# Performance work log

Measured on AMD Instinct MI355X. Metric: run time of the kernel, lower is better.

The kernel has to match this reference:

```python
import jax, jax.numpy as jnp
import numpy as np

B, Q, K, D, H = 2, 2048, 2048, 1024, 16
HD = D // H  # 64
EPS = 1e-6  # flax LayerNorm default epsilon


def setup_inputs() -> dict:
    key = jax.random.key(0)
    ks = jax.random.split(key, 12)
    s = 1.0 / np.sqrt(D)  # lecun_normal-like scale
    inputs_q = jax.random.normal(ks[0], (B, Q, D), jnp.float32)
    bias = jax.random.normal(ks[1], (B, 1, Q, K), jnp.float32)
    mask = jax.random.randint(ks[2], (B, 1, Q, K), 0, 2).astype(jnp.bool_)
    wq = jax.random.normal(ks[3], (D, H, HD), jnp.float32) * s
    wk = jax.random.normal(ks[4], (D, H, HD), jnp.float32) * s
    wv = jax.random.normal(ks[5], (D, H, HD), jnp.float32) * s
    bq = jnp.zeros((H, HD), jnp.float32)
    bk = jnp.zeros((H, HD), jnp.float32)
    bv = jnp.zeros((H, HD), jnp.float32)
    q_scale = jnp.ones((HD,), jnp.float32)
    k_scale = jnp.ones((HD,), jnp.float32)
    wo = jax.random.normal(ks[6], (H, HD, D), jnp.float32) * s
    bo = jnp.zeros((D,), jnp.float32)
    return dict(inputs_q=inputs_q, bias=bias, mask=mask, wq=wq, bq=bq,
                wk=wk, bk=bk, wv=wv, bv=bv, q_scale=q_scale, k_scale=k_scale,
                wo=wo, bo=bo)


def _layernorm_nobias(x, scale):
    # normalize over last axis (head_dim), no bias, like flax LayerNorm(use_bias=False)
    mean = jnp.mean(x, axis=-1, keepdims=True)
    var = jnp.mean(jnp.square(x - mean), axis=-1, keepdims=True)
    return (x - mean) * jax.lax.rsqrt(var + EPS) * scale


def reference(inputs_q, bias, mask, wq, bq, wk, bk, wv, bv, q_scale, k_scale, wo, bo):
    # QKV projections (self-attention: k and v inputs default to inputs_q)
    q = jnp.einsum('bqd,dhe->bqhe', inputs_q, wq) + bq  # [B,Q,H,HD]
    k = jnp.einsum('bkd,dhe->bkhe', inputs_q, wk) + bk  # [B,K,H,HD]
    v = jnp.einsum('bkd,dhe->bkhe', inputs_q, wv) + bv  # [B,K,H,HD]
    # optional QK layernorm (normalize_qk=True)
    q = _layernorm_nobias(q, q_scale)
    k = _layernorm_nobias(k, k_scale)
    # attention weights
    q = q / jnp.sqrt(jnp.asarray(q.shape[-1], q.dtype))
    attn = jnp.einsum('bqhe,bkhe->bhqk', q, k)  # [B,H,Q,K]
    attn = attn + bias
    big_neg = jnp.finfo(q.dtype).min
    attn = jnp.where(mask, attn, big_neg)
    attn = jax.nn.softmax(attn.astype(jnp.float32), axis=-1).astype(q.dtype)
    # weighted values + output projection
    x = jnp.einsum('bhqk,bkhe->bqhe', attn, v)  # [B,Q,H,HD]
    out = jnp.einsum('bqhe,heo->bqo', x, wo) + bo  # [B,Q,D]
    return out
```

## Files before the change

### kernel.cpp

```cpp
#include <hip/hip_runtime.h>
#include <cstdint>
#include <cstddef>

typedef __bf16 bf16_t;
typedef __bf16 bf16x8 __attribute__((ext_vector_type(8)));
typedef __bf16 bf16x4 __attribute__((ext_vector_type(4)));
typedef _Float16 f16_t;
typedef _Float16 f16x4 __attribute__((ext_vector_type(4)));
typedef float f32x4 __attribute__((ext_vector_type(4)));

constexpr int BB = 2, SS = 2048, DD = 1024, HH = 16, HDIM = 64;
constexpr int BS = BB * SS;
constexpr float LOG2E = 1.4426950408889634f;

__device__ __forceinline__ void glds16(const void* g, void* l) {
  __builtin_amdgcn_global_load_lds((const __attribute__((address_space(1))) void*)g,
                                   (__attribute__((address_space(3))) void*)l, 16, 0, 0);
}

__global__ __launch_bounds__(256) void prep_fused(
    const float* __restrict__ x, const float* __restrict__ wq, const float* __restrict__ wk,
    const float* __restrict__ wv, const float* __restrict__ wo, const float* __restrict__ bias,
    const int* __restrict__ mask, bf16_t* __restrict__ xb, bf16_t* __restrict__ wqkv_t,
    bf16_t* __restrict__ wo_t, bf16_t* __restrict__ bmq) {
  __shared__ float tile[64][65];
  int bid = blockIdx.x;
  int t = threadIdx.x;
  if (bid < 4096) {
    int i = bid * 256 + t;
    float4 v = ((const float4*)x)[i];
    union { bf16_t h[4]; uint2 u; } o;
    o.h[0] = (bf16_t)v.x; o.h[1] = (bf16_t)v.y; o.h[2] = (bf16_t)v.z; o.h[3] = (bf16_t)v.w;
    ((uint2*)xb)[i] = o.u;
  } else if (bid < 5120) {
    int id = bid - 4096;
    int which = id >> 8, tr = (id >> 4) & 15, tc = id & 15;
    const float* src = (which == 0) ? wq : (which == 1) ? wk : (which == 2) ? wv : wo;
    bf16_t* dst = (which < 3) ? wqkv_t : wo_t;
    int noff = (which < 3) ? which * 1024 : 0;
#pragma unroll
    for (int p = 0; p < 4; ++p) {
      int e = (p * 256 + t) * 4;
      int r = e >> 6, c = e & 63;
      float4 v = *(const float4*)&src[(size_t)(tr * 64 + r) * 1024 + tc * 64 + c];
      tile[r][c] = v.x; tile[r][c + 1] = v.y; tile[r][c + 2] = v.z; tile[r][c + 3] = v.w;
    }
    __syncthreads();
#pragma unroll
    for (int p = 0; p < 4; ++p) {
      int e = (p * 256 + t) * 4;
      int r = e >> 6, c = e & 63;
      union { bf16_t h[4]; uint2 u; } o;
#pragma unroll
      for (int j = 0; j < 4; ++j) o.h[j] = (bf16_t)tile[c + j][r];
      *(uint2*)&dst[(size_t)(noff + tc * 64 + r) * 1024 + tr * 64 + c] = o.u;
    }
  } else {
    int i = (bid - 5120) * 256 + t;
    float4 b0 = ((const float4*)bias)[i * 2];
    float4 b1 = ((const float4*)bias)[i * 2 + 1];
    int4 m0 = ((const int4*)mask)[i * 2];
    int4 m1 = ((const int4*)mask)[i * 2 + 1];
    union { bf16_t h[8]; uint4 u; } o;
    o.h[0] = (bf16_t)(m0.x ? b0.x * LOG2E - 8.0f : -2.0e38f);
    o.h[1] = (bf16_t)(m0.y ? b0.y * LOG2E - 8.0f : -2.0e38f);
    o.h[2] = (bf16_t)(m0.z ? b0.z * LOG2E - 8.0f : -2.0e38f);
    o.h[3] = (bf16_t)(m0.w ? b0.w * LOG2E - 8.0f : -2.0e38f);
    o.h[4] = (bf16_t)(m1.x ? b1.x * LOG2E - 8.0f : -2.0e38f);
    o.h[5] = (bf16_t)(m1.y ? b1.y * LOG2E - 8.0f : -2.0e38f);
    o.h[6] = (bf16_t)(m1.z ? b1.z * LOG2E - 8.0f : -2.0e38f);
    o.h[7] = (bf16_t)(m1.w ? b1.w * LOG2E - 8.0f : -2.0e38f);
    ((uint4*)bmq)[i] = o.u;
  }
}

template <bool OUT_F32>
__global__ __launch_bounds__(256) void gemm_bt(const bf16_t* __restrict__ A,
                                               const bf16_t* __restrict__ Bt,
                                               bf16_t* __restrict__ Cb, float* __restrict__ Cf,
                                               const float* __restrict__ bias, int M, int N,
                                               int Kd) {
  __shared__ __align__(16) bf16_t As[128][32];
  __shared__ __align__(16) bf16_t Bs[128][32];
  int tid = threadIdx.x;
  int lane = tid & 63, w = tid >> 6;
  int lo = lane & 15, quad = lane >> 4;
  int wm = w >> 1, wn = w & 1;
  int m0 = blockIdx.y * 128, n0 = blockIdx.x * 128;
  int srow = lane >> 2;
  int scol = (lane & 3) * 8;
  f32x4 acc[4][4] = {};
  for (int kk = 0; kk < Kd; kk += 32) {
#pragma unroll
    for (int t = 0; t < 2; ++t) {
      int rb = (w * 2 + t) * 16;
      glds16(&A[(size_t)(m0 + rb + srow) * Kd + kk + scol], &As[rb][0]);
      glds16(&Bt[(size_t)(n0 + rb + srow) * Kd + kk + scol], &Bs[rb][0]);
    }
    asm volatile("s_waitcnt vmcnt(0)" ::: "memory");
    __syncthreads();
    bf16x8 am[4], bn[4];
#pragma unroll
    for (int i = 0; i < 4; ++i) am[i] = *(const bf16x8*)&As[wm * 64 + i * 16 + lo][quad * 8];
#pragma unroll
    for (int i = 0; i < 4; ++i) bn[i] = *(const bf16x8*)&Bs[wn * 64 + i * 16 + lo][quad * 8];
#pragma unroll
    for (int mi = 0; mi < 4; ++mi)
#pragma unroll
      for (int ni = 0; ni < 4; ++ni)
        acc[mi][ni] = __builtin_amdgcn_mfma_f32_16x16x32_bf16(am[mi], bn[ni], acc[mi][ni], 0, 0, 0);
    __syncthreads();
  }
#pragma unroll
  for (int mi = 0; mi < 4; ++mi) {
#pragma unroll
    for (int ni = 0; ni < 4; ++ni) {
#pragma unroll
      for (int r = 0; r < 4; ++r) {
        int row = m0 + wm * 64 + mi * 16 + quad * 4 + r;
        int col = n0 + wn * 64 + ni * 16 + lo;
        float v = acc[mi][ni][r];
        if (OUT_F32)
          Cf[(size_t)row * N + col] = v + bias[col];
        else
          Cb[(size_t)row * N + col] = (bf16_t)v;
      }
    }
  }
}

__global__ __launch_bounds__(256) void postqkv(const bf16_t* __restrict__ Cqkv,
                                               const float* __restrict__ bq,
                                               const float* __restrict__ bk,
                                               const float* __restrict__ bv,
                                               const float* __restrict__ q_scale,
                                               const float* __restrict__ k_scale,
                                               bf16_t* __restrict__ qb, bf16_t* __restrict__ kb,
                                               f16_t* __restrict__ vt) {
  __shared__ float tile[64][65];
  int bid = blockIdx.x;
  int t = threadIdx.x;
  if (bid < 32768) {
    int mode = bid >> 14;
    int vec = (bid & 16383) * 4 + (t >> 6);
    int lane = t & 63;
    int bs = vec >> 4, h = vec & 15;
    int b = bs >> 11, s = bs & 2047;
    const float* badd = (mode == 0) ? bq : bk;
    float x = (float)Cqkv[(size_t)bs * 3072 + mode * 1024 + h * 64 + lane] + badd[h * 64 + lane];
    float sum = x;
#pragma unroll
    for (int off = 32; off >= 1; off >>= 1) sum += __shfl_xor(sum, off, 64);
    float mean = sum * (1.0f / 64.0f);
    float d = x - mean;
    float vs = d * d;
#pragma unroll
    for (int off = 32; off >= 1; off >>= 1) vs += __shfl_xor(vs, off, 64);
    float var = vs * (1.0f / 64.0f);
    const float* sc = (mode == 0) ? q_scale : k_scale;
    float y = d * rsqrtf(var + 1e-6f) * sc[lane];
    if (mode == 0) y *= 0.125f * LOG2E;
    bf16_t* dst = (mode == 0) ? qb : kb;
    dst[(size_t)((b * 16 + h) * 2048 + s) * 64 + lane] = (bf16_t)y;
  } else {
    int id2 = bid - 32768;
    int st = id2 & 31, h = (id2 >> 5) & 15, b = id2 >> 9;
#pragma unroll
    for (int p = 0; p < 2; ++p) {
      int e = (p * 256 + t) * 8;
      int r = e >> 6, c = e & 63;
      bf16x8 v8 = *(const bf16x8*)&Cqkv[(size_t)(b * SS + st * 64 + r) * 3072 + 2048 + h * 64 + c];
#pragma unroll
      for (int j = 0; j < 8; ++j) tile[r][c + j] = (float)v8[j] + bv[h * 64 + c + j];
    }
    __syncthreads();
#pragma unroll
    for (int p = 0; p < 2; ++p) {
      int e = (p * 256 + t) * 8;
      int r = e >> 6, c = e & 63;
      union { f16_t h[8]; uint4 u; } o;
#pragma unroll
      for (int j = 0; j < 8; ++j) o.h[j] = (f16_t)tile[c + j][r];
      *(uint4*)&vt[(size_t)((b * HH + h) * HDIM + r) * SS + st * 64 + c] = o.u;
    }
  }
}

__global__ __launch_bounds__(256) void attn_kernel(const bf16_t* __restrict__ qb,
                                                   const bf16_t* __restrict__ kb,
                                                   const f16_t* __restrict__ vt,
                                                   const bf16_t* __restrict__ bmq,
                                                   bf16_t* __restrict__ xout) {
  __shared__ __align__(16) bf16_t Ks[64][72];
  __shared__ __align__(16) f16_t Vs[64][72];
  __shared__ __align__(16) bf16_t Bm[128][72];
  int tid = threadIdx.x;
  int lane = tid & 63, w = tid >> 6;
  int lo = lane & 15, quad = lane >> 4;
  int qt = blockIdx.x, h = blockIdx.y, b = blockIdx.z;
  size_t headoff = (size_t)(b * HH + h) * SS * HDIM;
  int q0b = qt * 128;
  int q0 = q0b + w * 32;
  const bf16_t* kbase = kb + headoff;
  const f16_t* vbase = vt + headoff;
  const bf16_t* bmbase = bmq + (size_t)b * SS * SS;

  bf16x8 bqf[2][2];
#pragma unroll
  for (int qg = 0; qg < 2; ++qg)
#pragma unroll
    for (int ec = 0; ec < 2; ++ec)
      bqf[qg][ec] =
          *(const bf16x8*)&qb[headoff + (size_t)(q0 + qg * 16 + lo) * HDIM + ec * 32 + quad * 8];

  f16x4 ones;
#pragma unroll
  for (int j = 0; j < 4; ++j) ones[j] = (f16_t)1.0f;

  f32x4 ot[2][4] = {};
  f32x4 lacc[2] = {};

  for (int kt = 0; kt < SS / 64; ++kt) {
    int k0 = kt * 64;
#pragma unroll
    for (int p = 0; p < 2; ++p) {
      int idx = (p * 256 + tid) * 8;
      int r = idx >> 6, c = idx & 63;
      *(uint4*)&Ks[r][c] = *(const uint4*)&kbase[(size_t)(k0 + r) * HDIM + c];
      *(uint4*)&Vs[r][c] = *(const uint4*)&vbase[(size_t)r * SS + k0 + c];
    }
#pragma unroll
    for (int p = 0; p < 4; ++p) {
      int idx = (p * 256 + tid) * 8;
      int r = idx >> 6, c = idx & 63;
      *(uint4*)&Bm[r][c] = *(const uint4*)&bmbase[(size_t)(q0b + r) * SS + k0 + c];
    }
    __syncthreads();

    bf16x8 ka[4][2];
#pragma unroll
    for (int mb = 0; mb < 4; ++mb)
#pragma unroll
      for (int ec = 0; ec < 2; ++ec)
        ka[mb][ec] = *(const bf16x8*)&Ks[mb * 16 + lo][ec * 32 + quad * 8];

    f16x4 pf[2][4];
#pragma unroll
    for (int qg = 0; qg < 2; ++qg) {
#pragma unroll
      for (int mb = 0; mb < 4; ++mb) {
        bf16x4 bm4 = *(const bf16x4*)&Bm[w * 32 + qg * 16 + lo][mb * 16 + quad * 4];
        f32x4 s;
#pragma unroll
        for (int r = 0; r < 4; ++r) s[r] = (float)bm4[r];
        s = __builtin_amdgcn_mfma_f32_16x16x32_bf16(ka[mb][0], bqf[qg][0], s, 0, 0, 0);
        s = __builtin_amdgcn_mfma_f32_16x16x32_bf16(ka[mb][1], bqf[qg][1], s, 0, 0, 0);
#pragma unroll
        for (int r = 0; r < 4; ++r) pf[qg][mb][r] = (f16_t)__builtin_amdgcn_exp2f(s[r]);
      }
    }

#pragma unroll
    for (int mb = 0; mb < 4; ++mb) {
#pragma unroll
      for (int eb = 0; eb < 4; ++eb) {
        f16x4 va = *(const f16x4*)&Vs[eb * 16 + lo][mb * 16 + quad * 4];
#pragma unroll
        for (int qg = 0; qg < 2; ++qg)
          ot[qg][eb] = __builtin_amdgcn_mfma_f32_16x16x16f16(va, pf[qg][mb], ot[qg][eb], 0, 0, 0);
      }
#pragma unroll
      for (int qg = 0; qg < 2; ++qg)
        lacc[qg] = __builtin_amdgcn_mfma_f32_16x16x16f16(ones, pf[qg][mb], lacc[qg], 0, 0, 0);
    }
    __syncthreads();
  }

#pragma unroll
  for (int qg = 0; qg < 2; ++qg) {
    float rl = 1.0f / lacc[qg][0];
    int q = q0 + qg * 16 + lo;
#pragma unroll
    for (int eb = 0; eb < 4; ++eb) {
      union { bf16_t h4[4]; uint2 u; } o;
#pragma unroll
      for (int r = 0; r < 4; ++r) o.h4[r] = (bf16_t)(ot[qg][eb][r] * rl);
      *(uint2*)&xout[(size_t)(b * SS + q) * DD + h * 64 + eb * 16 + quad * 4] = o.u;
    }
  }
}

extern "C" void kernel_launch(void* const* d_in, const int* in_sizes, int n_in, void* d_out,
                              int out_size, void* d_ws, size_t ws_size, hipStream_t stream) {
  const float* inputs_q = (const float*)d_in[0];
  const float* bias = (const float*)d_in[1];
  const int* mask = (const int*)d_in[2];
  const float* wq = (const float*)d_in[3];
  const float* bq = (const float*)d_in[4];
  const float* wk = (const float*)d_in[5];
  const float* bk = (const float*)d_in[6];
  const float* wv = (const float*)d_in[7];
  const float* bv = (const float*)d_in[8];
  const float* q_scale = (const float*)d_in[9];
  const float* k_scale = (const float*)d_in[10];
  const float* wo = (const float*)d_in[11];
  const float* bo = (const float*)d_in[12];
  float* out = (float*)d_out;

  char* ws = (char*)d_ws;
  bf16_t* wo_t   = (bf16_t*)(ws);
  bf16_t* bmq    = (bf16_t*)(ws + ((size_t)2 << 20));
  bf16_t* cqkv   = (bf16_t*)(ws + ((size_t)19 << 20));
  bf16_t* xattn  = (bf16_t*)(ws + ((size_t)19 << 20));
  bf16_t* xb     = (bf16_t*)(ws + ((size_t)43 << 20));
  bf16_t* qb2    = (bf16_t*)(ws + ((size_t)43 << 20));
  bf16_t* wqkv_t = (bf16_t*)(ws + ((size_t)51 << 20));
  bf16_t* kb2    = (bf16_t*)(ws + ((size_t)51 << 20));
  f16_t*  vtb    = (f16_t*)(ws + ((size_t)59 << 20));

  prep_fused<<<9216, 256, 0, stream>>>(inputs_q, wq, wk, wv, wo, bias, mask, xb, wqkv_t, wo_t, bmq);
  gemm_bt<false><<<dim3(24, 32), 256, 0, stream>>>(xb, wqkv_t, cqkv, nullptr, nullptr, BS, 3072, DD);
  postqkv<<<33792, 256, 0, stream>>>(cqkv, bq, bk, bv, q_scale, k_scale, qb2, kb2, vtb);
  attn_kernel<<<dim3(SS / 128, HH, BB), 256, 0, stream>>>(qb2, kb2, vtb, bmq, xattn);
  gemm_bt<true><<<dim3(8, 32), 256, 0, stream>>>(xattn, wo_t, nullptr, out, bo, BS, 1024, DD);
}
```

Baseline: 300.7 us.

## Precompute exp(bias)*mask multiplier, double-buffer attention tiles, swizzle K/V layouts

The bias+mask term is now precomputed as an fp16 multiplicative factor exp2(bias*log2e-8), or zero where masked. It is stored in MFMA fragment order so the attention kernel loads it straight into registers and multiplies the exponentiated scores, replacing an LDS bias tile and its adds. K and V tiles are double-buffered in LDS using direct global-to-LDS loads with XOR-swizzled layouts, written that way by postqkv, to avoid bank conflicts and overlap loads with compute. Scores are clamped before exp2 to keep fp16 finite, and the output GEMM uses 64-wide N tiles for more blocks. The factored exponent shifts numerics: underflow of the precomputed factor and the clamp could change results for extreme values.

```diff
diff --git a/kernel.cpp b/kernel.cpp
--- a/kernel.cpp
+++ b/kernel.cpp
@@ -7,6 +7,7 @@
 typedef __bf16 bf16x4 __attribute__((ext_vector_type(4)));
 typedef _Float16 f16_t;
 typedef _Float16 f16x4 __attribute__((ext_vector_type(4)));
+typedef _Float16 f16x2 __attribute__((ext_vector_type(2)));
 typedef float f32x4 __attribute__((ext_vector_type(4)));
 
 constexpr int BB = 2, SS = 2048, DD = 1024, HH = 16, HDIM = 64;
@@ -22,8 +23,10 @@
     const float* __restrict__ x, const float* __restrict__ wq, const float* __restrict__ wk,
     const float* __restrict__ wv, const float* __restrict__ wo, const float* __restrict__ bias,
     const int* __restrict__ mask, bf16_t* __restrict__ xb, bf16_t* __restrict__ wqkv_t,
-    bf16_t* __restrict__ wo_t, bf16_t* __restrict__ bmq) {
-  __shared__ float tile[64][65];
+    bf16_t* __restrict__ wo_t, f16_t* __restrict__ vmq) {
+  __shared__ __align__(16) char smem[18432];
+  float (*tile)[65] = (float(*)[65])smem;
+  f16_t (*btile)[72] = (f16_t(*)[72])smem;
   int bid = blockIdx.x;
   int t = threadIdx.x;
   if (bid < 4096) {
@@ -56,69 +59,93 @@
       *(uint2*)&dst[(size_t)(noff + tc * 64 + r) * 1024 + tr * 64 + c] = o.u;
     }
   } else {
-    int i = (bid - 5120) * 256 + t;
-    float4 b0 = ((const float4*)bias)[i * 2];
-    float4 b1 = ((const float4*)bias)[i * 2 + 1];
-    int4 m0 = ((const int4*)mask)[i * 2];
-    int4 m1 = ((const int4*)mask)[i * 2 + 1];
-    union { bf16_t h[8]; uint4 u; } o;
-    o.h[0] = (bf16_t)(m0.x ? b0.x * LOG2E - 8.0f : -2.0e38f);
-    o.h[1] = (bf16_t)(m0.y ? b0.y * LOG2E - 8.0f : -2.0e38f);
-    o.h[2] = (bf16_t)(m0.z ? b0.z * LOG2E - 8.0f : -2.0e38f);
-    o.h[3] = (bf16_t)(m0.w ? b0.w * LOG2E - 8.0f : -2.0e38f);
-    o.h[4] = (bf16_t)(m1.x ? b1.x * LOG2E - 8.0f : -2.0e38f);
-    o.h[5] = (bf16_t)(m1.y ? b1.y * LOG2E - 8.0f : -2.0e38f);
-    o.h[6] = (bf16_t)(m1.z ? b1.z * LOG2E - 8.0f : -2.0e38f);
-    o.h[7] = (bf16_t)(m1.w ? b1.w * LOG2E - 8.0f : -2.0e38f);
-    ((uint4*)bmq)[i] = o.u;
-  }
-}
-
-template <bool OUT_F32>
+    int id = bid - 5120;
+    int b = id >> 9, qt = (id >> 5) & 15, kt = id & 31;
+    size_t base_in = ((size_t)(b * 2048 + qt * 128)) * 2048 + kt * 64;
+#pragma unroll
+    for (int p = 0; p < 4; ++p) {
+      int c = p * 256 + t;
+      int qr = c >> 3, k8 = (c & 7) * 8;
+      const float* bp = &bias[base_in + (size_t)qr * 2048 + k8];
+      const int* mp = &mask[base_in + (size_t)qr * 2048 + k8];
+      float4 b0 = *(const float4*)bp;
+      float4 b1 = *(const float4*)(bp + 4);
+      int4 m0 = *(const int4*)mp;
+      int4 m1 = *(const int4*)(mp + 4);
+      union { f16_t h[8]; uint4 u; } o;
+      o.h[0] = m0.x ? (f16_t)__builtin_amdgcn_exp2f(b0.x * LOG2E - 8.0f) : (f16_t)0.0f;
+      o.h[1] = m0.y ? (f16_t)__builtin_amdgcn_exp2f(b0.y * LOG2E - 8.0f) : (f16_t)0.0f;
+      o.h[2] = m0.z ? (f16_t)__builtin_amdgcn_exp2f(b0.z * LOG2E - 8.0f) : (f16_t)0.0f;
+      o.h[3] = m0.w ? (f16_t)__builtin_amdgcn_exp2f(b0.w * LOG2E - 8.0f) : (f16_t)0.0f;
+      o.h[4] = m1.x ? (f16_t)__builtin_amdgcn_exp2f(b1.x * LOG2E - 8.0f) : (f16_t)0.0f;
+      o.h[5] = m1.y ? (f16_t)__builtin_amdgcn_exp2f(b1.y * LOG2E - 8.0f) : (f16_t)0.0f;
+      o.h[6] = m1.z ? (f16_t)__builtin_amdgcn_exp2f(b1.z * LOG2E - 8.0f) : (f16_t)0.0f;
+      o.h[7] = m1.w ? (f16_t)__builtin_amdgcn_exp2f(b1.w * LOG2E - 8.0f) : (f16_t)0.0f;
+      *(uint4*)&btile[qr][k8] = o.u;
+    }
+    __syncthreads();
+    int w = t >> 6, lane = t & 63, lo = lane & 15, quad = lane >> 4;
+    size_t obase = ((size_t)(((b * 16 + qt) * 32 + kt) * 16)) * 64;
+#pragma unroll
+    for (int j = 0; j < 4; ++j) {
+      int row = w * 32 + (j >> 1) * 16 + lo;
+      int mbl = 2 * (j & 1);
+      union { f16_t h[8]; uint4 u; } o;
+#pragma unroll
+      for (int e = 0; e < 8; ++e)
+        o.h[e] = btile[row][(mbl + (e >> 2)) * 16 + quad * 4 + (e & 3)];
+      ((uint4*)vmq)[obase + (w * 4 + j) * 64 + lane] = o.u;
+    }
+  }
+}
+
+template <bool OUT_F32, int BNT>
 __global__ __launch_bounds__(256) void gemm_bt(const bf16_t* __restrict__ A,
                                                const bf16_t* __restrict__ Bt,
                                                bf16_t* __restrict__ Cb, float* __restrict__ Cf,
                                                const float* __restrict__ bias, int M, int N,
                                                int Kd) {
+  constexpr int WNW = BNT / 2;
+  constexpr int NFR = WNW / 16;
   __shared__ __align__(16) bf16_t As[128][32];
-  __shared__ __align__(16) bf16_t Bs[128][32];
+  __shared__ __align__(16) bf16_t Bs[BNT][32];
   int tid = threadIdx.x;
   int lane = tid & 63, w = tid >> 6;
   int lo = lane & 15, quad = lane >> 4;
   int wm = w >> 1, wn = w & 1;
-  int m0 = blockIdx.y * 128, n0 = blockIdx.x * 128;
+  int m0 = blockIdx.y * 128, n0 = blockIdx.x * BNT;
   int srow = lane >> 2;
   int scol = (lane & 3) * 8;
-  f32x4 acc[4][4] = {};
+  f32x4 acc[4][NFR] = {};
   for (int kk = 0; kk < Kd; kk += 32) {
 #pragma unroll
     for (int t = 0; t < 2; ++t) {
       int rb = (w * 2 + t) * 16;
       glds16(&A[(size_t)(m0 + rb + srow) * Kd + kk + scol], &As[rb][0]);
-      glds16(&Bt[(size_t)(n0 + rb + srow) * Kd + kk + scol], &Bs[rb][0]);
+      if (rb < BNT) glds16(&Bt[(size_t)(n0 + rb + srow) * Kd + kk + scol], &Bs[rb][0]);
     }
     asm volatile("s_waitcnt vmcnt(0)" ::: "memory");
     __syncthreads();
-    bf16x8 am[4], bn[4];
+    bf16x8 am[4], bn[NFR];
 #pragma unroll
     for (int i = 0; i < 4; ++i) am[i] = *(const bf16x8*)&As[wm * 64 + i * 16 + lo][quad * 8];
 #pragma unroll
-    for (int i = 0; i < 4; ++i) bn[i] = *(const bf16x8*)&Bs[wn * 64 + i * 16 + lo][quad * 8];
+    for (int i = 0; i < NFR; ++i) bn[i] = *(const bf16x8*)&Bs[wn * WNW + i * 16 + lo][quad * 8];
 #pragma unroll
     for (int mi = 0; mi < 4; ++mi)
 #pragma unroll
-      for (int ni = 0; ni < 4; ++ni)
+      for (int ni = 0; ni < NFR; ++ni)
         acc[mi][ni] = __builtin_amdgcn_mfma_f32_16x16x32_bf16(am[mi], bn[ni], acc[mi][ni], 0, 0, 0);
     __syncthreads();
   }
 #pragma unroll
   for (int mi = 0; mi < 4; ++mi) {
 #pragma unroll
-    for (int ni = 0; ni < 4; ++ni) {
+    for (int ni = 0; ni < NFR; ++ni) {
 #pragma unroll
       for (int r = 0; r < 4; ++r) {
         int row = m0 + wm * 64 + mi * 16 + quad * 4 + r;
-        int col = n0 + wn * 64 + ni * 16 + lo;
+        int col = n0 + wn * WNW + ni * 16 + lo;
         float v = acc[mi][ni][r];
         if (OUT_F32)
           Cf[(size_t)row * N + col] = v + bias[col];
@@ -161,7 +188,8 @@
     float y = d * rsqrtf(var + 1e-6f) * sc[lane];
     if (mode == 0) y *= 0.125f * LOG2E;
     bf16_t* dst = (mode == 0) ? qb : kb;
-    dst[(size_t)((b * 16 + h) * 2048 + s) * 64 + lane] = (bf16_t)y;
+    int el = (mode == 0) ? lane : ((((lane >> 3) ^ (s & 7)) << 3) | (lane & 7));
+    dst[(size_t)((b * 16 + h) * 2048 + s) * 64 + el] = (bf16_t)y;
   } else {
     int id2 = bid - 32768;
     int st = id2 & 31, h = (id2 >> 5) & 15, b = id2 >> 9;
@@ -181,7 +209,8 @@
       union { f16_t h[8]; uint4 u; } o;
 #pragma unroll
       for (int j = 0; j < 8; ++j) o.h[j] = (f16_t)tile[c + j][r];
-      *(uint4*)&vt[(size_t)((b * HH + h) * HDIM + r) * SS + st * 64 + c] = o.u;
+      *(uint4*)&vt[(size_t)((b * HH + h) * HDIM + r) * SS + st * 64 +
+                   ((((c >> 3) ^ (r & 7)) << 3))] = o.u;
     }
   }
 }
@@ -189,21 +218,20 @@
 __global__ __launch_bounds__(256) void attn_kernel(const bf16_t* __restrict__ qb,
                                                    const bf16_t* __restrict__ kb,
                                                    const f16_t* __restrict__ vt,
-                                                   const bf16_t* __restrict__ bmq,
+                                                   const f16_t* __restrict__ vmq,
                                                    bf16_t* __restrict__ xout) {
-  __shared__ __align__(16) bf16_t Ks[64][72];
-  __shared__ __align__(16) f16_t Vs[64][72];
-  __shared__ __align__(16) bf16_t Bm[128][72];
+  __shared__ __align__(16) bf16_t Ks[2][64][64];
+  __shared__ __align__(16) f16_t Vs[2][64][64];
   int tid = threadIdx.x;
   int lane = tid & 63, w = tid >> 6;
   int lo = lane & 15, quad = lane >> 4;
   int qt = blockIdx.x, h = blockIdx.y, b = blockIdx.z;
   size_t headoff = (size_t)(b * HH + h) * SS * HDIM;
-  int q0b = qt * 128;
-  int q0 = q0b + w * 32;
+  int q0 = qt * 128 + w * 32;
   const bf16_t* kbase = kb + headoff;
   const f16_t* vbase = vt + headoff;
-  const bf16_t* bmbase = bmq + (size_t)b * SS * SS;
+  const uint4* vmbase =
+      (const uint4*)vmq + ((size_t)((b * 16 + qt) * 32) * 16 + w * 4) * 64 + lane;
 
   bf16x8 bqf[2][2];
 #pragma unroll
@@ -220,43 +248,61 @@
   f32x4 ot[2][4] = {};
   f32x4 lacc[2] = {};
 
+  union VM { uint4 u; f16x4 q[2]; };
+  VM vr[4];
+
+#pragma unroll
+  for (int tt = 0; tt < 2; ++tt) {
+    int i = w * 2 + tt;
+    int r = i * 8 + (lane >> 3);
+    glds16(&kbase[(size_t)r * 64 + ((lane & 7) << 3)], &Ks[0][i * 8][0]);
+    glds16(&vbase[(size_t)r * SS + ((lane & 7) << 3)], &Vs[0][i * 8][0]);
+  }
+#pragma unroll
+  for (int j = 0; j < 4; ++j) vr[j].u = vmbase[j * 64];
+  asm volatile("s_waitcnt vmcnt(0)" ::: "memory");
+  __syncthreads();
+
+#pragma unroll 2
   for (int kt = 0; kt < SS / 64; ++kt) {
-    int k0 = kt * 64;
-#pragma unroll
-    for (int p = 0; p < 2; ++p) {
-      int idx = (p * 256 + tid) * 8;
-      int r = idx >> 6, c = idx & 63;
-      *(uint4*)&Ks[r][c] = *(const uint4*)&kbase[(size_t)(k0 + r) * HDIM + c];
-      *(uint4*)&Vs[r][c] = *(const uint4*)&vbase[(size_t)r * SS + k0 + c];
-    }
-#pragma unroll
-    for (int p = 0; p < 4; ++p) {
-      int idx = (p * 256 + tid) * 8;
-      int r = idx >> 6, c = idx & 63;
-      *(uint4*)&Bm[r][c] = *(const uint4*)&bmbase[(size_t)(q0b + r) * SS + k0 + c];
-    }
-    __syncthreads();
+    int cur = kt & 1;
+    VM vn[4];
+    if (kt < SS / 64 - 1) {
+      int k0n = (kt + 1) * 64;
+#pragma unroll
+      for (int tt = 0; tt < 2; ++tt) {
+        int i = w * 2 + tt;
+        int r = i * 8 + (lane >> 3);
+        glds16(&kbase[(size_t)(k0n + r) * 64 + ((lane & 7) << 3)], &Ks[cur ^ 1][i * 8][0]);
+        glds16(&vbase[(size_t)r * SS + k0n + ((lane & 7) << 3)], &Vs[cur ^ 1][i * 8][0]);
+      }
+#pragma unroll
+      for (int j = 0; j < 4; ++j) vn[j].u = vmbase[(size_t)(kt + 1) * 1024 + j * 64];
+    }
 
     bf16x8 ka[4][2];
 #pragma unroll
-    for (int mb = 0; mb < 4; ++mb)
+    for (int mb = 0; mb < 4; ++mb) {
+      const char* krow = (const char*)&Ks[cur][mb * 16 + lo][0];
 #pragma unroll
       for (int ec = 0; ec < 2; ++ec)
-        ka[mb][ec] = *(const bf16x8*)&Ks[mb * 16 + lo][ec * 32 + quad * 8];
+        ka[mb][ec] = *(const bf16x8*)(krow + ((((ec << 2) | quad) ^ (lo & 7)) << 4));
+    }
 
     f16x4 pf[2][4];
 #pragma unroll
     for (int qg = 0; qg < 2; ++qg) {
 #pragma unroll
       for (int mb = 0; mb < 4; ++mb) {
-        bf16x4 bm4 = *(const bf16x4*)&Bm[w * 32 + qg * 16 + lo][mb * 16 + quad * 4];
-        f32x4 s;
-#pragma unroll
-        for (int r = 0; r < 4; ++r) s[r] = (float)bm4[r];
+        f32x4 s = {};
         s = __builtin_amdgcn_mfma_f32_16x16x32_bf16(ka[mb][0], bqf[qg][0], s, 0, 0, 0);
         s = __builtin_amdgcn_mfma_f32_16x16x32_bf16(ka[mb][1], bqf[qg][1], s, 0, 0, 0);
-#pragma unroll
-        for (int r = 0; r < 4; ++r) pf[qg][mb][r] = (f16_t)__builtin_amdgcn_exp2f(s[r]);
+        f16x4 p4;
+        p4[0] = (f16_t)__builtin_amdgcn_exp2f(fminf(s[0], 15.0f));
+        p4[1] = (f16_t)__builtin_amdgcn_exp2f(fminf(s[1], 15.0f));
+        p4[2] = (f16_t)__builtin_amdgcn_exp2f(fminf(s[2], 15.0f));
+        p4[3] = (f16_t)__builtin_amdgcn_exp2f(fminf(s[3], 15.0f));
+        pf[qg][mb] = p4 * vr[qg * 2 + (mb >> 1)].q[mb & 1];
       }
     }
 
@@ -264,7 +310,9 @@
     for (int mb = 0; mb < 4; ++mb) {
 #pragma unroll
       for (int eb = 0; eb < 4; ++eb) {
-        f16x4 va = *(const f16x4*)&Vs[eb * 16 + lo][mb * 16 + quad * 4];
+        const char* vrow = (const char*)&Vs[cur][eb * 16 + lo][0];
+        f16x4 va = *(const f16x4*)(vrow + (((((mb << 1) | (quad >> 1)) ^ (lo & 7)) << 4) |
+                                           ((quad & 1) << 3)));
 #pragma unroll
         for (int qg = 0; qg < 2; ++qg)
           ot[qg][eb] = __builtin_amdgcn_mfma_f32_16x16x16f16(va, pf[qg][mb], ot[qg][eb], 0, 0, 0);
@@ -273,7 +321,13 @@
       for (int qg = 0; qg < 2; ++qg)
         lacc[qg] = __builtin_amdgcn_mfma_f32_16x16x16f16(ones, pf[qg][mb], lacc[qg], 0, 0, 0);
     }
-    __syncthreads();
+
+    asm volatile("s_waitcnt vmcnt(0)" ::: "memory");
+    __syncthreads();
+    if (kt < SS / 64 - 1) {
+#pragma unroll
+      for (int j = 0; j < 4; ++j) vr[j] = vn[j];
+    }
   }
 
 #pragma unroll
@@ -309,7 +363,7 @@
 
   char* ws = (char*)d_ws;
   bf16_t* wo_t   = (bf16_t*)(ws);
-  bf16_t* bmq    = (bf16_t*)(ws + ((size_t)2 << 20));
+  f16_t*  vmq    = (f16_t*)(ws + ((size_t)2 << 20));
   bf16_t* cqkv   = (bf16_t*)(ws + ((size_t)19 << 20));
   bf16_t* xattn  = (bf16_t*)(ws + ((size_t)19 << 20));
   bf16_t* xb     = (bf16_t*)(ws + ((size_t)43 << 20));
@@ -318,9 +372,10 @@
   bf16_t* kb2    = (bf16_t*)(ws + ((size_t)51 << 20));
   f16_t*  vtb    = (f16_t*)(ws + ((size_t)59 << 20));
 
-  prep_fused<<<9216, 256, 0, stream>>>(inputs_q, wq, wk, wv, wo, bias, mask, xb, wqkv_t, wo_t, bmq);
-  gemm_bt<false><<<dim3(24, 32), 256, 0, stream>>>(xb, wqkv_t, cqkv, nullptr, nullptr, BS, 3072, DD);
+  prep_fused<<<6144, 256, 0, stream>>>(inputs_q, wq, wk, wv, wo, bias, mask, xb, wqkv_t, wo_t, vmq);
+  gemm_bt<false, 128><<<dim3(24, 32), 256, 0, stream>>>(xb, wqkv_t, cqkv, nullptr, nullptr, BS,
+                                                        3072, DD);
   postqkv<<<33792, 256, 0, stream>>>(cqkv, bq, bk, bv, q_scale, k_scale, qb2, kb2, vtb);
-  attn_kernel<<<dim3(SS / 128, HH, BB), 256, 0, stream>>>(qb2, kb2, vtb, bmq, xattn);
-  gemm_bt<true><<<dim3(8, 32), 256, 0, stream>>>(xattn, wo_t, nullptr, out, bo, BS, 1024, DD);
-}
+  attn_kernel<<<dim3(SS / 128, HH, BB), 256, 0, stream>>>(qb2, kb2, vtb, vmq, xattn);
+  gemm_bt<true, 64><<<dim3(16, 32), 256, 0, stream>>>(xattn, wo_t, nullptr, out, bo, BS, 1024, DD);
+}
```

Result: no change. 303.7 us (+1.0%).
